# Kernel tuning notes

Measured on AMD Instinct MI355X. Metric: run time of the kernel, lower is better.

## Reference

```python
import jax, jax.numpy as jnp
import numpy as np

NUM_HEADS = 16


def setup_inputs() -> dict:
    key = jax.random.key(0)
    k1, k2, k3, k4, k5 = jax.random.split(key, 5)
    B, N, C = 4, 1370, 1024
    s = 0.02
    return {
        "tokens": jax.random.normal(k1, (B, N, C), jnp.float32),
        "qkv_w": jax.random.normal(k2, (3 * C, C), jnp.float32) * s,
        "qkv_b": jax.random.normal(k3, (3 * C,), jnp.float32) * s,
        "proj_w": jax.random.normal(k4, (C, C), jnp.float32) * s,
        "proj_b": jax.random.normal(k5, (C,), jnp.float32) * s,
    }


def reference(tokens, qkv_w, qkv_b, proj_w, proj_b):
    B, N, C = tokens.shape
    H = NUM_HEADS
    c = C // H
    scale = c ** (-0.5)
    # qkv projection: [B,N,3C] -> [3,B,H,N,c]
    qkv = tokens @ qkv_w.T + qkv_b
    qkv = qkv.reshape(B, N, 3, H, c).transpose(2, 0, 3, 1, 4)
    q, k, v = qkv[0], qkv[1], qkv[2]
    q = q * scale
    attn = jnp.einsum("bhqc,bhkc->bhqk", q, k)  # [B,H,N,N]
    w = jax.nn.softmax(attn, axis=-1)
    out = jnp.einsum("bhqk,bhkc->bhqc", w, v)  # [B,H,N,c]
    out = out.transpose(0, 2, 1, 3).reshape(B, N, C)
    return out @ proj_w.T + proj_b
```

## Files before the change

### kernel.cpp

```cpp
#include <hip/hip_runtime.h>
#include <hip/hip_bf16.h>

typedef short s16x8 __attribute__((ext_vector_type(8)));
typedef float f32x4 __attribute__((ext_vector_type(4)));
typedef float f32x16 __attribute__((ext_vector_type(16)));
typedef unsigned short u16;
typedef unsigned int   u32;
typedef u16 u16x4 __attribute__((ext_vector_type(4)));

#define SEQ  1370
#define CH   1024
#define NH   16
#define HD   64
#define BN   5480
#define MPAD 5504
#define NPAD 1408
#define NQT  43
#define NKT64 22

#define QSCALE 0.18033688f


__device__ __forceinline__ u16 f2bf(float f){
  union { float f; unsigned u; } v; v.f = f;
  unsigned u = v.u;
  return (u16)((u + 0x7FFFu + ((u >> 16) & 1u)) >> 16);
}

__device__ __forceinline__ u32 cvt_pk_bf16(float lo, float hi){
  u32 r;
  asm("v_cvt_pk_bf16_f32 %0, %1, %2" : "=v"(r) : "v"(lo), "v"(hi));
  return r;
}

#define GLOAD16(gp, lp) __builtin_amdgcn_global_load_lds( \
    (const __attribute__((address_space(1))) void*)(gp), \
    (__attribute__((address_space(3))) void*)(lp), 16, 0, 0)

__global__ __launch_bounds__(256) void k_cast_tokens(const float* __restrict__ in, u16* __restrict__ out){
  int i8 = (blockIdx.x * 256 + threadIdx.x) * 8;
  if(i8 >= MPAD*CH) return;
  int row = i8 >> 10;
  s16x8 o = {0,0,0,0,0,0,0,0};
  if(row < BN){
    f32x4 a = *reinterpret_cast<const f32x4*>(in + i8);
    f32x4 b = *reinterpret_cast<const f32x4*>(in + i8 + 4);
#pragma unroll
    for(int j=0;j<4;j++){ o[j] = (short)f2bf(a[j]); o[4+j] = (short)f2bf(b[j]); }
  }
  *reinterpret_cast<s16x8*>(out + i8) = o;
}

__global__ __launch_bounds__(256) void k_cast(const float* __restrict__ in, u16* __restrict__ out, int n){
  int i8 = (blockIdx.x * 256 + threadIdx.x) * 8;
  if(i8 >= n) return;
  f32x4 a = *reinterpret_cast<const f32x4*>(in + i8);
  f32x4 b = *reinterpret_cast<const f32x4*>(in + i8 + 4);
  s16x8 o;
#pragma unroll
  for(int j=0;j<4;j++){ o[j] = (short)f2bf(a[j]); o[4+j] = (short)f2bf(b[j]); }
  *reinterpret_cast<s16x8*>(out + i8) = o;
}

template<int MODE, int NT>
__global__ __launch_bounds__(256,4) void k_gemm128(
    const u16* __restrict__ A, const u16* __restrict__ Bw, const float* __restrict__ bias,
    u16* __restrict__ q, u16* __restrict__ kk_, u16* __restrict__ vv, float* __restrict__ out)
{
  constexpr int NF = NT/32;
  __shared__ u16 As[128*64];
  __shared__ u16 Bs[NT*64];
  const int t = threadIdx.x;
  const int lane = t & 63;
  const int w = t >> 6;
  const int wm = w >> 1, wn = w & 1;
  const int g = lane >> 4, lr = lane & 15;

  const int bid = blockIdx.x;
  const int xcd = bid & 7, idx = bid >> 3;
  const int xr = xcd & 3, yr = xcd >> 2;
  constexpr int YLOC = (MODE == 0) ? 12 : 8;
  const int x = xr*11 + idx % 11;
  const int y = yr*YLOC + idx / 11;
  if(x >= MPAD/128) return;
  const int m0 = x*128, n0 = y*NT;

  const int swc = ((t & 7) ^ ((t >> 3) & 7)) * 8;
  const u16* ga0 = A  + (size_t)(m0 + (t >> 3)) * 1024 + swc;
  const u16* gb0 = Bw + (size_t)(n0 + (t >> 3)) * 1024 + swc;

  f32x4 z = {0.f,0.f,0.f,0.f};
  f32x4 acc[4][NF];
#pragma unroll
  for(int mf=0;mf<4;mf++)
#pragma unroll
    for(int nf=0;nf<NF;nf++) acc[mf][nf] = z;

  for(int k0 = 0; k0 < 1024; k0 += 64){
#pragma unroll
    for(int j=0;j<4;j++)
      GLOAD16(ga0 + k0 + j*32*1024, As + j*2048 + w*512);
#pragma unroll
    for(int j=0;j<NF;j++)
      GLOAD16(gb0 + k0 + j*32*1024, Bs + j*2048 + w*512);
    __syncthreads();
#pragma unroll
    for(int kk=0; kk<2; kk++){
      s16x8 af[4], bf[NF];
#pragma unroll
      for(int mf = 0; mf < 4; mf++)
        af[mf] = *reinterpret_cast<const s16x8*>(&As[(wm*64 + mf*16 + lr)*64 + ((kk*4+g) ^ (lr&7))*8]);
#pragma unroll
      for(int nf = 0; nf < NF; nf++)
        bf[nf] = *reinterpret_cast<const s16x8*>(&Bs[(wn*16*NF + nf*16 + lr)*64 + ((kk*4+g) ^ (lr&7))*8]);
#pragma unroll
      for(int mf = 0; mf < 4; mf++)
#pragma unroll
        for(int nf = 0; nf < NF; nf++)
          acc[mf][nf] = __builtin_amdgcn_mfma_f32_16x16x32_bf16(af[mf], bf[nf], acc[mf][nf], 0,0,0);
    }
    __syncthreads();
  }

#pragma unroll
  for(int mf = 0; mf < 4; mf++){
#pragma unroll
    for(int nf = 0; nf < NF; nf++){
      int colc = n0 + wn*16*NF + nf*16 + lr;
      float bb = bias[colc];
      if constexpr (MODE == 0){
        int tt = colc >> 10, h = (colc >> 6) & 15, cc = colc & 63;
        const int rowb = m0 + wm*64 + mf*16 + g*4;
        if(tt == 2){
          int b = rowb / SEQ;
          int nb = rowb - b*SEQ;
          if(rowb + 3 < BN && nb + 4 <= SEQ && (nb & 3) == 0){
            int bh = b*NH + h;
            int ktv = nb >> 6, kh = (nb >> 4) & 3, hiv = (nb >> 3) & 1;
            int e0 = nb & 7;
            int dtv = cc >> 5, colr = cc & 31;
            u16x4 ov;
#pragma unroll
            for(int r=0;r<4;r++) ov[r] = f2bf(acc[mf][nf][r] + bb);
            *reinterpret_cast<u16x4*>(vv +
              (size_t)((((bh*22 + ktv)*4 + kh)*2 + dtv)*2 + hiv)*256 + colr*8 + e0) = ov;
          } else {
#pragma unroll
            for(int r = 0; r < 4; r++){
              int row = rowb + r;
              if(row >= BN) continue;
              int b2 = row / SEQ, n = row - b2*SEQ;
              int bh = b2*NH + h;
              int ktv = n >> 6, kh = (n >> 4) & 3, hiv = (n >> 3) & 1, e = n & 7;
              int dtv = cc >> 5, colr = cc & 31;
              vv[(size_t)((((bh*22 + ktv)*4 + kh)*2 + dtv)*2 + hiv)*256 + colr*8 + e]
                = f2bf(acc[mf][nf][r] + bb);
            }
          }
        } else {
#pragma unroll
          for(int r = 0; r < 4; r++){
            int row = rowb + r;
            if(row >= BN) continue;
            int b = row / SEQ, n = row - b*SEQ;
            int bh = b*NH + h;
            int gg = n >> 5, colr = n & 31;
            int dtv = cc >> 4, hiq = (cc >> 3) & 1, e = cc & 7;
            size_t fidx = (size_t)(((bh*44 + gg)*4 + dtv)*2 + hiq)*256 + colr*8 + e;
            float v = acc[mf][nf][r] + bb;
            if(tt == 0) q  [fidx] = f2bf(v * QSCALE);
            else        kk_[fidx] = f2bf(v);
          }
        }
      } else {
#pragma unroll
        for(int r = 0; r < 4; r++){
          int row = m0 + wm*64 + mf*16 + g*4 + r;
          if(row >= BN) continue;
          out[(size_t)row * CH + colc] = acc[mf][nf][r] + bb;
        }
      }
    }
  }
}

__global__ __launch_bounds__(256,3) void k_attn9(
    const u16* __restrict__ Qf, const u16* __restrict__ Kf,
    const u16* __restrict__ Vf, u16* __restrict__ O)
{
  __shared__ u16 Kl[2][4096];
  __shared__ u16 Vl[2][4096];
  const int bid = blockIdx.x;
  const int swz = (bid & 7)*88 + (bid >> 3);
  const int bh = swz / 11;
  const int qg = swz - bh*11;
  const int w = threadIdx.x >> 6;
  int qt = qg*4 + w;
  const bool wr = (qt < NQT);
  if(!wr) qt = NQT - 1;
  const int lane = threadIdx.x & 63;
  const int col = lane & 31;
  const int hi  = lane >> 5;
  const int n0  = qt * 32;
  const int lofs = hi*256 + col*8;

  s16x8 qf[4];
  {
    const u16* qfb = Qf + (size_t)(bh*44 + qt)*2048 + lofs;
#pragma unroll
    for(int dt=0; dt<4; dt++)
      qf[dt] = *reinterpret_cast<const s16x8*>(qfb + dt*512);
  }
  const u16* kfb = Kf + (size_t)bh*44*2048;
  const u16* vfb = Vf + (size_t)bh*22*4096;

#define STAGE_T(KT, CB) { \
  const u16* gk_ = kfb + (size_t)(KT)*4096 + w*1024 + lane*8; \
  const u16* gv_ = vfb + (size_t)(KT)*4096 + w*1024 + lane*8; \
  GLOAD16(gk_,       &Kl[CB][w*1024]); \
  GLOAD16(gk_ + 512, &Kl[CB][w*1024 + 512]); \
  GLOAD16(gv_,       &Vl[CB][w*1024]); \
  GLOAD16(gv_ + 512, &Vl[CB][w*1024 + 512]); }

  f32x16 accO[2];
  f32x16 accL;
#pragma unroll
  for(int i=0;i<16;i++){ accO[0][i]=0.f; accO[1][i]=0.f; accL[i]=0.f; }
  const s16x8 onesf = {(short)0x3F80,(short)0x3F80,(short)0x3F80,(short)0x3F80,
                       (short)0x3F80,(short)0x3F80,(short)0x3F80,(short)0x3F80};

  STAGE_T(0, 0);
  asm volatile("s_waitcnt vmcnt(0)" ::: "memory");
  __builtin_amdgcn_s_barrier();

  for(int kt = 0; kt < NKT64; kt++){
    const int kj0 = kt * 64;
    const int cur = kt & 1;
    if(kt + 1 < NKT64) STAGE_T(kt + 1, cur^1);
    f32x16 St[2];
    __builtin_amdgcn_s_setprio(1);
#pragma unroll
    for(int s=0;s<2;s++){
#pragma unroll
      for(int i=0;i<16;i++) St[s][i]=0.f;
#pragma unroll
      for(int dt=0;dt<4;dt++){
        s16x8 kf = *reinterpret_cast<const s16x8*>(&Kl[cur][s*2048 + dt*512 + lofs]);
        St[s] = __builtin_amdgcn_mfma_f32_32x32x16_bf16(kf, qf[dt], St[s], 0,0,0);
      }
    }
    __builtin_amdgcn_s_setprio(0);
    float p[32];
    if(kj0 + 64 <= SEQ){
#pragma unroll
      for(int i=0;i<32;i++) p[i] = exp2f(St[i>>4][i&15]);
    } else {
#pragma unroll
      for(int s=0;s<2;s++)
#pragma unroll
        for(int r=0;r<16;r++){
          int k = kj0 + s*32 + (r&3) + 8*(r>>2) + 4*hi;
          p[s*16+r] = (k < SEQ) ? exp2f(St[s][r]) : 0.f;
        }
    }
    union PF { u32 w[4]; s16x8 v; } pf[4];
#pragma unroll
    for(int s=0;s<2;s++){
#pragma unroll
      for(int hh=0; hh<2; hh++){
        const int b0 = s*16 + hh*8;
        u32 w0 = cvt_pk_bf16(p[b0+0], p[b0+1]);
        u32 w1 = cvt_pk_bf16(p[b0+2], p[b0+3]);
        u32 w2 = cvt_pk_bf16(p[b0+4], p[b0+5]);
        u32 w3 = cvt_pk_bf16(p[b0+6], p[b0+7]);
        auto r02 = __builtin_amdgcn_permlane32_swap(w0, w2, false, false);
        auto r13 = __builtin_amdgcn_permlane32_swap(w1, w3, false, false);
        pf[s*2+hh].w[0] = r02[0];
        pf[s*2+hh].w[1] = r13[0];
        pf[s*2+hh].w[2] = r02[1];
        pf[s*2+hh].w[3] = r13[1];
      }
    }
    __builtin_amdgcn_s_setprio(1);
#pragma unroll
    for(int kh=0; kh<4; kh++){
#pragma unroll
      for(int dt=0; dt<2; dt++){
        s16x8 vf = *reinterpret_cast<const s16x8*>(&Vl[cur][(kh*2+dt)*512 + lofs]);
        accO[dt] = __builtin_amdgcn_mfma_f32_32x32x16_bf16(vf, pf[kh].v, accO[dt], 0,0,0);
      }
      accL = __builtin_amdgcn_mfma_f32_32x32x16_bf16(onesf, pf[kh].v, accL, 0,0,0);
    }
    __builtin_amdgcn_s_setprio(0);
    asm volatile("s_waitcnt vmcnt(0)" ::: "memory");
    __builtin_amdgcn_s_barrier();
  }

  const int n = n0 + col;
  if(wr && n < SEQ){
    float inv = 1.0f / accL[0];
    const int b = bh >> 4, h = bh & 15;
    u16* orow = O + ((size_t)(b*SEQ + n))*CH + h*HD;
#pragma unroll
    for(int dt=0; dt<2; dt++)
#pragma unroll
      for(int qd=0; qd<4; qd++){
        u16x4 ov;
#pragma unroll
        for(int j=0;j<4;j++) ov[j] = f2bf(accO[dt][qd*4+j]*inv);
        *reinterpret_cast<u16x4*>(orow + dt*32 + qd*8 + hi*4) = ov;
      }
  }
}

extern "C" void kernel_launch(void* const* d_in, const int* in_sizes, int n_in,
                              void* d_out, int out_size, void* d_ws, size_t ws_size,
                              hipStream_t stream)
{
  const float* tokens = (const float*)d_in[0];
  const float* qkv_w  = (const float*)d_in[1];
  const float* qkv_b  = (const float*)d_in[2];
  const float* proj_w = (const float*)d_in[3];
  const float* proj_b = (const float*)d_in[4];
  float* out = (float*)d_out;

  char* ws = (char*)d_ws;
  u16* Xbf   = (u16*)(ws);
  u16* Wqkv  = (u16*)(ws + 11272192);
  u16* Wproj = (u16*)(ws + 17563648);
  u16* Qfb   = (u16*)(ws + 19660800);
  u16* Kfb   = (u16*)(ws + 31195136);
  u16* Vfb   = (u16*)(ws + 42729472);
  u16* AttO  = (u16*)(ws + 65798144);

  k_cast_tokens<<<dim3((MPAD*CH)/2048), 256, 0, stream>>>(tokens, Xbf);
  k_cast<<<dim3((3*CH*CH)/2048), 256, 0, stream>>>(qkv_w, Wqkv, 3*CH*CH);
  k_cast<<<dim3((CH*CH)/2048),   256, 0, stream>>>(proj_w, Wproj, CH*CH);

  k_gemm128<0,128><<<dim3(1056), 256, 0, stream>>>(Xbf, Wqkv, qkv_b, Qfb, Kfb, Vfb, nullptr);
  k_attn9<<<dim3(704), 256, 0, stream>>>(Qfb, Kfb, Vfb, AttO);
  k_gemm128<1,64><<<dim3(704), 256, 0, stream>>>(AttO, Wproj, proj_b, nullptr, nullptr, nullptr, out);
}
```

Measured before the change: 156.6 us.

## Software-pipeline attention loop so next tile's QK overlaps current softmax/PV

Splits K and V staging into separate macros and unrolls the key-tile loop by two. The QK^T score MFMAs for tile kt+1 are issued alongside the exp/convert/PV work for tile kt, with staggered K and V prefetches into the double buffers. The goal is to hide exp and permlane latency behind matrix-core work and to issue loads earlier. In exchange, a second set of score accumulators stays live, which raises register pressure under the 3-blocks-per-CU launch bound and could cause spills.

```diff
diff --git a/kernel.cpp b/kernel.cpp
--- a/kernel.cpp
+++ b/kernel.cpp
@@ -184,7 +184,7 @@
   }
 }
 
-__global__ __launch_bounds__(256,3) void k_attn9(
+__global__ __launch_bounds__(256,3) void k_attn11(
     const u16* __restrict__ Qf, const u16* __restrict__ Kf,
     const u16* __restrict__ Vf, u16* __restrict__ O)
 {
@@ -214,11 +214,13 @@
   const u16* kfb = Kf + (size_t)bh*44*2048;
   const u16* vfb = Vf + (size_t)bh*22*4096;
 
-#define STAGE_T(KT, CB) { \
+#define STAGE_K(KT, CB) { \
   const u16* gk_ = kfb + (size_t)(KT)*4096 + w*1024 + lane*8; \
+  GLOAD16(gk_,       &Kl[CB][w*1024]); \
+  GLOAD16(gk_ + 512, &Kl[CB][w*1024 + 512]); }
+
+#define STAGE_V(KT, CB) { \
   const u16* gv_ = vfb + (size_t)(KT)*4096 + w*1024 + lane*8; \
-  GLOAD16(gk_,       &Kl[CB][w*1024]); \
-  GLOAD16(gk_ + 512, &Kl[CB][w*1024 + 512]); \
   GLOAD16(gv_,       &Vl[CB][w*1024]); \
   GLOAD16(gv_ + 512, &Vl[CB][w*1024 + 512]); }
 
@@ -229,69 +231,84 @@
   const s16x8 onesf = {(short)0x3F80,(short)0x3F80,(short)0x3F80,(short)0x3F80,
                        (short)0x3F80,(short)0x3F80,(short)0x3F80,(short)0x3F80};
 
-  STAGE_T(0, 0);
+#define QK(St2, KT) { \
+  __builtin_amdgcn_s_setprio(1); \
+  _Pragma("unroll") \
+  for(int s_=0;s_<2;s_++){ \
+    _Pragma("unroll") for(int i_=0;i_<16;i_++) St2[s_][i_]=0.f; \
+    _Pragma("unroll") \
+    for(int dt_=0;dt_<4;dt_++){ \
+      s16x8 kf_ = *reinterpret_cast<const s16x8*>(&Kl[(KT)&1][s_*2048 + dt_*512 + lofs]); \
+      St2[s_] = __builtin_amdgcn_mfma_f32_32x32x16_bf16(kf_, qf[dt_], St2[s_], 0,0,0); \
+    } \
+  } \
+  __builtin_amdgcn_s_setprio(0); }
+
+#define SMPV(St2, KT) { \
+  const int kj0_ = (KT)*64; \
+  float p[32]; \
+  if(kj0_ + 64 <= SEQ){ \
+    _Pragma("unroll") for(int i_=0;i_<32;i_++) p[i_] = exp2f(St2[i_>>4][i_&15]); \
+  } else { \
+    _Pragma("unroll") \
+    for(int s_=0;s_<2;s_++) \
+      _Pragma("unroll") \
+      for(int r_=0;r_<16;r_++){ \
+        int k_ = kj0_ + s_*32 + (r_&3) + 8*(r_>>2) + 4*hi; \
+        p[s_*16+r_] = (k_ < SEQ) ? exp2f(St2[s_][r_]) : 0.f; \
+      } \
+  } \
+  union PF { u32 w[4]; s16x8 v; } pf[4]; \
+  _Pragma("unroll") \
+  for(int s_=0;s_<2;s_++){ \
+    _Pragma("unroll") \
+    for(int hh_=0; hh_<2; hh_++){ \
+      const int b0_ = s_*16 + hh_*8; \
+      u32 w0_ = cvt_pk_bf16(p[b0_+0], p[b0_+1]); \
+      u32 w1_ = cvt_pk_bf16(p[b0_+2], p[b0_+3]); \
+      u32 w2_ = cvt_pk_bf16(p[b0_+4], p[b0_+5]); \
+      u32 w3_ = cvt_pk_bf16(p[b0_+6], p[b0_+7]); \
+      auto r02_ = __builtin_amdgcn_permlane32_swap(w0_, w2_, false, false); \
+      auto r13_ = __builtin_amdgcn_permlane32_swap(w1_, w3_, false, false); \
+      pf[s_*2+hh_].w[0] = r02_[0]; \
+      pf[s_*2+hh_].w[1] = r13_[0]; \
+      pf[s_*2+hh_].w[2] = r02_[1]; \
+      pf[s_*2+hh_].w[3] = r13_[1]; \
+    } \
+  } \
+  __builtin_amdgcn_s_setprio(1); \
+  _Pragma("unroll") \
+  for(int kh_=0; kh_<4; kh_++){ \
+    _Pragma("unroll") \
+    for(int dt_=0; dt_<2; dt_++){ \
+      s16x8 vf_ = *reinterpret_cast<const s16x8*>(&Vl[(KT)&1][(kh_*2+dt_)*512 + lofs]); \
+      accO[dt_] = __builtin_amdgcn_mfma_f32_32x32x16_bf16(vf_, pf[kh_].v, accO[dt_], 0,0,0); \
+    } \
+    accL = __builtin_amdgcn_mfma_f32_32x32x16_bf16(onesf, pf[kh_].v, accL, 0,0,0); \
+  } \
+  __builtin_amdgcn_s_setprio(0); }
+
+  f32x16 StA[2], StB[2];
+
+  STAGE_K(0, 0);
+  STAGE_K(1, 1);
+  STAGE_V(0, 0);
   asm volatile("s_waitcnt vmcnt(0)" ::: "memory");
   __builtin_amdgcn_s_barrier();
-
-  for(int kt = 0; kt < NKT64; kt++){
-    const int kj0 = kt * 64;
-    const int cur = kt & 1;
-    if(kt + 1 < NKT64) STAGE_T(kt + 1, cur^1);
-    f32x16 St[2];
-    __builtin_amdgcn_s_setprio(1);
-#pragma unroll
-    for(int s=0;s<2;s++){
-#pragma unroll
-      for(int i=0;i<16;i++) St[s][i]=0.f;
-#pragma unroll
-      for(int dt=0;dt<4;dt++){
-        s16x8 kf = *reinterpret_cast<const s16x8*>(&Kl[cur][s*2048 + dt*512 + lofs]);
-        St[s] = __builtin_amdgcn_mfma_f32_32x32x16_bf16(kf, qf[dt], St[s], 0,0,0);
-      }
-    }
-    __builtin_amdgcn_s_setprio(0);
-    float p[32];
-    if(kj0 + 64 <= SEQ){
-#pragma unroll
-      for(int i=0;i<32;i++) p[i] = exp2f(St[i>>4][i&15]);
-    } else {
-#pragma unroll
-      for(int s=0;s<2;s++)
-#pragma unroll
-        for(int r=0;r<16;r++){
-          int k = kj0 + s*32 + (r&3) + 8*(r>>2) + 4*hi;
-          p[s*16+r] = (k < SEQ) ? exp2f(St[s][r]) : 0.f;
-        }
-    }
-    union PF { u32 w[4]; s16x8 v; } pf[4];
-#pragma unroll
-    for(int s=0;s<2;s++){
-#pragma unroll
-      for(int hh=0; hh<2; hh++){
-        const int b0 = s*16 + hh*8;
-        u32 w0 = cvt_pk_bf16(p[b0+0], p[b0+1]);
-        u32 w1 = cvt_pk_bf16(p[b0+2], p[b0+3]);
-        u32 w2 = cvt_pk_bf16(p[b0+4], p[b0+5]);
-        u32 w3 = cvt_pk_bf16(p[b0+6], p[b0+7]);
-        auto r02 = __builtin_amdgcn_permlane32_swap(w0, w2, false, false);
-        auto r13 = __builtin_amdgcn_permlane32_swap(w1, w3, false, false);
-        pf[s*2+hh].w[0] = r02[0];
-        pf[s*2+hh].w[1] = r13[0];
-        pf[s*2+hh].w[2] = r02[1];
-        pf[s*2+hh].w[3] = r13[1];
-      }
-    }
-    __builtin_amdgcn_s_setprio(1);
-#pragma unroll
-    for(int kh=0; kh<4; kh++){
-#pragma unroll
-      for(int dt=0; dt<2; dt++){
-        s16x8 vf = *reinterpret_cast<const s16x8*>(&Vl[cur][(kh*2+dt)*512 + lofs]);
-        accO[dt] = __builtin_amdgcn_mfma_f32_32x32x16_bf16(vf, pf[kh].v, accO[dt], 0,0,0);
-      }
-      accL = __builtin_amdgcn_mfma_f32_32x32x16_bf16(onesf, pf[kh].v, accL, 0,0,0);
-    }
-    __builtin_amdgcn_s_setprio(0);
+  QK(StA, 0);
+  __builtin_amdgcn_s_barrier();
+
+  for(int kt = 0; kt < NKT64; kt += 2){
+    if(kt + 2 < NKT64) STAGE_K(kt + 2, kt & 1);
+    STAGE_V(kt + 1, (kt + 1) & 1);
+    QK(StB, kt + 1);
+    SMPV(StA, kt);
+    asm volatile("s_waitcnt vmcnt(0)" ::: "memory");
+    __builtin_amdgcn_s_barrier();
+    if(kt + 3 < NKT64) STAGE_K(kt + 3, (kt + 3) & 1);
+    if(kt + 2 < NKT64) STAGE_V(kt + 2, kt & 1);
+    if(kt + 2 < NKT64) QK(StA, kt + 2);
+    SMPV(StB, kt + 1);
     asm volatile("s_waitcnt vmcnt(0)" ::: "memory");
     __builtin_amdgcn_s_barrier();
   }
@@ -338,6 +355,6 @@
   k_cast<<<dim3((CH*CH)/2048),   256, 0, stream>>>(proj_w, Wproj, CH*CH);
 
   k_gemm128<0,128><<<dim3(1056), 256, 0, stream>>>(Xbf, Wqkv, qkv_b, Qfb, Kfb, Vfb, nullptr);
-  k_attn9<<<dim3(704), 256, 0, stream>>>(Qfb, Kfb, Vfb, AttO);
+  k_attn11<<<dim3(704), 256, 0, stream>>>(Qfb, Kfb, Vfb, AttO);
   k_gemm128<1,64><<<dim3(704), 256, 0, stream>>>(AttO, Wproj, proj_b, nullptr, nullptr, nullptr, out);
 }
```

Result: slower. 167.2 us (+6.8%).
